# Kernel optimization log

Measured on AMD Instinct MI355X. Metric: run time of the kernel, lower is better.

Reference implementation:

```python
import jax, jax.numpy as jnp
import numpy as np

B = 256
NUM_ROUTES = 32 * 6 * 6  # 1152
NUM_CAPS = 10
OUT_CH = 16
IN_CH = 8


def squash(x, axis=-1):
    sq = jnp.sum(x * x, axis=axis, keepdims=True)
    return sq * x / ((1.0 + sq) * jnp.sqrt(sq))


def conv2d(x, w, b, stride):
    y = jax.lax.conv_general_dilated(
        x, w, window_strides=(stride, stride), padding='VALID',
        dimension_numbers=('NCHW', 'OIHW', 'NCHW'))
    return y + b[None, :, None, None]


def setup_inputs() -> dict:
    key = jax.random.key(0)
    ks = jax.random.split(key, 12)
    data = jax.random.normal(ks[0], (B, 1, 28, 28), dtype=jnp.float32)
    conv1_w = jax.random.normal(ks[1], (256, 1, 9, 9), dtype=jnp.float32) * 0.1
    conv1_b = jax.random.normal(ks[2], (256,), dtype=jnp.float32) * 0.01
    # 8 primary-capsule convs, each 256->32, k9 s2 (stacked)
    pc_w = jax.random.normal(ks[3], (8, 32, 256, 9, 9), dtype=jnp.float32) * 0.02
    pc_b = jax.random.normal(ks[4], (8, 32), dtype=jnp.float32) * 0.01
    # DigitCaps routing weights (torch.randn init)
    W_dc = jax.random.normal(ks[5], (NUM_ROUTES, NUM_CAPS, OUT_CH, IN_CH), dtype=jnp.float32)
    dec_w1 = jax.random.normal(ks[6], (160, 512), dtype=jnp.float32) * 0.05
    dec_b1 = jnp.zeros((512,), dtype=jnp.float32)
    dec_w2 = jax.random.normal(ks[7], (512, 1024), dtype=jnp.float32) * 0.05
    dec_b2 = jnp.zeros((1024,), dtype=jnp.float32)
    dec_w3 = jax.random.normal(ks[8], (1024, 784), dtype=jnp.float32) * 0.05
    dec_b3 = jnp.zeros((784,), dtype=jnp.float32)
    return dict(data=data, conv1_w=conv1_w, conv1_b=conv1_b, pc_w=pc_w, pc_b=pc_b,
                W_dc=W_dc, dec_w1=dec_w1, dec_b1=dec_b1, dec_w2=dec_w2,
                dec_b2=dec_b2, dec_w3=dec_w3, dec_b3=dec_b3)


def capsnet_forward(data, conv1_w, conv1_b, pc_w, pc_b, W_dc,
                    dec_w1, dec_b1, dec_w2, dec_b2, dec_w3, dec_b3):
    bsz = data.shape[0]
    # ConvLayer: [B,1,28,28] -> [B,256,20,20]
    x = jax.nn.relu(conv2d(data, conv1_w, conv1_b, 1))
    # PrimaryCaps: 8 independent convs fused into one 256-out conv then split
    # [B,256,6,6] viewed as [B,8,32,6,6] matches torch.stack(u, dim=1)
    u = conv2d(x, pc_w.reshape(256, 256, 9, 9), pc_b.reshape(256), 2)
    u = u.reshape(bsz, NUM_ROUTES, IN_CH)  # [B,1152,8]
    u = squash(u)
    # DigitCaps: u_hat[b,r,c,o] = sum_i W[r,c,o,i] * u[b,r,i]
    u_hat = jnp.einsum('rcoi,bri->brco', W_dc, u)  # [B,1152,10,16]
    b_ij = jnp.zeros((NUM_ROUTES, NUM_CAPS), dtype=u_hat.dtype)
    num_iterations = 3
    v = None
    for it in range(num_iterations):
        c_ij = jax.nn.softmax(b_ij, axis=0)            # softmax over routes
        s_j = jnp.einsum('rc,brco->bco', c_ij, u_hat)  # [B,10,16]
        v = squash(s_j, axis=-1)
        if it < num_iterations - 1:
            a_ij = jnp.einsum('brco,bco->rc', u_hat, v) / bsz  # mean over batch
            b_ij = b_ij + a_ij
    output = v[..., None]  # [B,10,16,1]
    # Decoder
    classes = jnp.sqrt(jnp.sum(output ** 2, axis=2))   # [B,10,1]
    classes = jax.nn.softmax(classes, axis=0)          # softmax over batch (as in source)
    idx = jnp.argmax(classes, axis=1)[:, 0]            # [B]
    masked = jnp.eye(NUM_CAPS, dtype=output.dtype)[idx]  # [B,10]
    t = (output * masked[:, :, None, None]).reshape(bsz, -1)  # [B,160]
    h = jax.nn.relu(t @ dec_w1 + dec_b1)
    h = jax.nn.relu(h @ dec_w2 + dec_b2)
    recon = jax.nn.sigmoid(h @ dec_w3 + dec_b3).reshape(bsz, 1, 28, 28)
    return output, recon, masked


def reference(data, conv1_w, conv1_b, pc_w, pc_b, W_dc,
              dec_w1, dec_b1, dec_w2, dec_b2, dec_w3, dec_b3):
    return capsnet_forward(data, conv1_w, conv1_b, pc_w, pc_b, W_dc,
                           dec_w1, dec_b1, dec_w2, dec_b2, dec_w3, dec_b3)
```

## Files before the change

### kernel.cpp

```cpp
#include <hip/hip_runtime.h>
#include <math.h>


typedef __attribute__((ext_vector_type(8))) short short8;
typedef __attribute__((ext_vector_type(4))) float f32x4;

__device__ __forceinline__ unsigned short f2bf(float x) {
  unsigned int u = __float_as_uint(x);
  unsigned int r = (u + 0x7fffu + ((u >> 16) & 1u)) >> 16;
  return (unsigned short)r;
}
__device__ __forceinline__ float bf2f(unsigned short h) {
  return __uint_as_float(((unsigned int)h) << 16);
}
__device__ __forceinline__ void gload16(const void* g, void* l) {
  __builtin_amdgcn_global_load_lds(
      (const __attribute__((address_space(1))) unsigned int*)g,
      (__attribute__((address_space(3))) unsigned int*)l, 16, 0, 0);
}
__device__ __forceinline__ float dot8(const float* w, float4 a, float4 b) {
  return w[0]*a.x + w[1]*a.y + w[2]*a.z + w[3]*a.w +
         w[4]*b.x + w[5]*b.y + w[6]*b.z + w[7]*b.w;
}

__global__ __launch_bounds__(320) void conv1_kernel(
    const float* __restrict__ data, const float* __restrict__ w1,
    const float* __restrict__ b1, unsigned short* __restrict__ xh,
    unsigned short* __restrict__ xl)
{
  const int bid = blockIdx.x;
  const int b   = bid >> 2;
  const int cog = bid & 3;
  __shared__ float img[784];
  __shared__ float wsm[81][64];
  const int t = threadIdx.x;
  for (int i = t; i < 784; i += 320) img[i] = data[b * 784 + i];
  for (int i = t; i < 64 * 81; i += 320) {
    int col = i / 81, k = i % 81;
    wsm[k][col] = w1[(cog * 64 + col) * 81 + k];
  }
  __syncthreads();
  const int cg = t & 15;
  const int oy = t >> 4;
  const int co0 = cog * 64 + cg * 4;
  float acc[4][20];
  #pragma unroll
  for (int i = 0; i < 4; i++) {
    float bv = b1[co0 + i];
    #pragma unroll
    for (int j = 0; j < 20; j++) acc[i][j] = bv;
  }
  for (int ky = 0; ky < 9; ky++) {
    float xr[28];
    const float4* rp = reinterpret_cast<const float4*>(&img[(oy + ky) * 28]);
    #pragma unroll
    for (int q = 0; q < 7; q++) {
      float4 v4 = rp[q];
      xr[q*4+0] = v4.x; xr[q*4+1] = v4.y; xr[q*4+2] = v4.z; xr[q*4+3] = v4.w;
    }
    #pragma unroll
    for (int kx = 0; kx < 9; kx++) {
      float4 wv = *reinterpret_cast<const float4*>(&wsm[ky * 9 + kx][cg * 4]);
      #pragma unroll
      for (int ox = 0; ox < 20; ox++) {
        float xv = xr[ox + kx];
        acc[0][ox] = fmaf(xv, wv.x, acc[0][ox]);
        acc[1][ox] = fmaf(xv, wv.y, acc[1][ox]);
        acc[2][ox] = fmaf(xv, wv.z, acc[2][ox]);
        acc[3][ox] = fmaf(xv, wv.w, acc[3][ox]);
      }
    }
  }
  #pragma unroll
  for (int ox = 0; ox < 20; ox++) {
    ushort4 hv, lv;
    float v0 = fmaxf(acc[0][ox], 0.f), v1 = fmaxf(acc[1][ox], 0.f);
    float v2 = fmaxf(acc[2][ox], 0.f), v3 = fmaxf(acc[3][ox], 0.f);
    hv.x = f2bf(v0); lv.x = f2bf(v0 - bf2f(hv.x));
    hv.y = f2bf(v1); lv.y = f2bf(v1 - bf2f(hv.y));
    hv.z = f2bf(v2); lv.z = f2bf(v2 - bf2f(hv.z));
    hv.w = f2bf(v3); lv.w = f2bf(v3 - bf2f(hv.w));
    const int pix = (b * 20 + oy) * 20 + ox;
    *(ushort4*)(xh + pix * 256 + co0) = hv;
    *(ushort4*)(xl + pix * 256 + co0) = lv;
  }
}

__global__ void wprep(const float* __restrict__ pw, unsigned short* __restrict__ wh,
                      unsigned short* __restrict__ wl)
{
  const int co = blockIdx.x;
  const int t  = threadIdx.x;
  __shared__ float slab[20736];
  for (int i = t; i < 20736; i += 256) slab[i] = pw[co * 20736 + i];
  __syncthreads();
  const int cc = t >> 5, ci5 = t & 31;
  for (int k = 0; k < 81; k++) {
    float x = slab[t * 81 + k];
    unsigned short h = f2bf(x);
    int dst = ((k * 8 + cc) * 256 + co) * 32 + ci5;
    wh[dst] = h;
    wl[dst] = f2bf(x - bf2f(h));
  }
}

__global__ __launch_bounds__(512) void conv2_mfma(
    const unsigned short* __restrict__ xh, const unsigned short* __restrict__ xl,
    const unsigned short* __restrict__ wh, const unsigned short* __restrict__ wl,
    float* __restrict__ part)
{
  extern __shared__ char lds[];
  const int t   = threadIdx.x;
  const int blk = blockIdx.x;
  const int mt  = blk % 72;
  const int kg  = blk / 72;
  const int m0  = mt * 128;
  const int lane = t & 63;
  const int w    = t >> 6;
  const int l15  = lane & 15, l4 = lane >> 4;
  const int mh = w >> 2, nw = w & 3;

  const int g0   = t ^ ((t >> 3) & 7);
  const int row0 = g0 >> 3, ch = g0 & 7;
  auto pixbase = [&](int pix) {
    int ab = pix / 36; int sp = pix - ab * 36;
    int oy = sp / 6;   int ox = sp - oy * 6;
    return ((ab * 20 + 2 * oy) * 20 + 2 * ox) * 256;
  };
  const int abase0 = pixbase(m0 + row0) + ch * 8;
  const int abase1 = pixbase(m0 + row0 + 64) + ch * 8;

  const int bofs = (nw * 64 + l15) * 32 + l4 * 8;

  f32x4 acc[4][4];
  #pragma unroll
  for (int i = 0; i < 4; i++)
    #pragma unroll
    for (int j = 0; j < 4; j++) acc[i][j] = (f32x4){0.f, 0.f, 0.f, 0.f};

  const int ky0 = kg * 3;

  auto stageA = [&](int buf, int xy, int ci0) {
    char* base = lds + buf * 32768;
    gload16(xh + abase0 + xy + ci0, base + t * 16);
    gload16(xh + abase1 + xy + ci0, base + 8192  + t * 16);
    gload16(xl + abase0 + xy + ci0, base + 16384 + t * 16);
    gload16(xl + abase1 + xy + ci0, base + 24576 + t * 16);
  };

  stageA(0, ky0 * 20 * 256, 0);
  int kyc = ky0, kxc = 0, cc2 = 0;
  #pragma unroll 1
  for (int s = 0; s < 108; ++s) {
    const int kkc = (kyc * 9 + kxc) * 8 + cc2 * 2;
    short8 b_h[4][2], b_l[4][2];
    #pragma unroll
    for (int ks = 0; ks < 2; ks++) {
      const unsigned short* bhp = wh + (kkc + ks) * 8192 + bofs;
      const unsigned short* blp = wl + (kkc + ks) * 8192 + bofs;
      #pragma unroll
      for (int nf = 0; nf < 4; nf++) {
        b_h[nf][ks] = *(const short8*)(bhp + nf * 512);
        b_l[nf][ks] = *(const short8*)(blp + nf * 512);
      }
    }
    cc2++; if (cc2 == 4) { cc2 = 0; kxc++; if (kxc == 9) { kxc = 0; kyc++; } }
    if (s < 107) {
      stageA((s + 1) % 3, (kyc * 20 + kxc) * 256, cc2 * 64);
      asm volatile("s_waitcnt vmcnt(20)" ::: "memory");
    } else {
      asm volatile("s_waitcnt vmcnt(16)" ::: "memory");
    }
    asm volatile("s_barrier" ::: "memory");

    char* base = lds + (s % 3) * 32768;
    #pragma unroll
    for (int ks = 0; ks < 2; ks++) {
      short8 a_h[4], a_l[4];
      #pragma unroll
      for (int mf = 0; mf < 4; mf++) {
        const int row = mh * 64 + mf * 16 + l15;
        const int off = ((row * 8 + ks * 4 + l4) ^ (row & 7)) << 4;
        a_h[mf] = *(const short8*)(base + off);
        a_l[mf] = *(const short8*)(base + 16384 + off);
      }
      __builtin_amdgcn_s_setprio(1);
      #pragma unroll
      for (int nf = 0; nf < 4; nf++)
        #pragma unroll
        for (int mf = 0; mf < 4; mf++) {
          f32x4 a = acc[mf][nf];
          a = __builtin_amdgcn_mfma_f32_16x16x32_bf16(a_h[mf], b_h[nf][ks], a, 0, 0, 0);
          a = __builtin_amdgcn_mfma_f32_16x16x32_bf16(a_l[mf], b_h[nf][ks], a, 0, 0, 0);
          a = __builtin_amdgcn_mfma_f32_16x16x32_bf16(a_h[mf], b_l[nf][ks], a, 0, 0, 0);
          acc[mf][nf] = a;
        }
      __builtin_amdgcn_s_setprio(0);
    }
  }

  float* pout = part + kg * 2359296;
  #pragma unroll
  for (int mf = 0; mf < 4; mf++)
    #pragma unroll
    for (int nf = 0; nf < 4; nf++) {
      const int co = nw * 64 + nf * 16 + l15;
      #pragma unroll
      for (int reg = 0; reg < 4; reg++) {
        const int pix = m0 + mh * 64 + mf * 16 + l4 * 4 + reg;
        const int b  = pix / 36;
        const int sp = pix - b * 36;
        pout[b * 9216 + co * 36 + sp] = acc[mf][nf][reg];
      }
    }
}

__global__ void combine_squash(const float* __restrict__ part,
                               const float* __restrict__ pb,
                               float* __restrict__ uT)
{
  const int id = blockIdx.x * 256 + threadIdx.x;
  const int b = id / 1152;
  const int r = id % 1152;
  const float* p0 = part + b * 9216 + r * 8;
  float v[8];
  #pragma unroll
  for (int i = 0; i < 8; i++) v[i] = p0[i] + p0[2359296 + i] + p0[4718592 + i];
  #pragma unroll
  for (int i = 0; i < 8; i++) v[i] += pb[(r * 8 + i) / 36];
  float sq = 0.f;
  #pragma unroll
  for (int i = 0; i < 8; i++) sq += v[i] * v[i];
  float scale = sq / ((1.f + sq) * sqrtf(sq));
  #pragma unroll
  for (int i = 0; i < 8; i++) uT[(r * 256 + b) * 8 + i] = v[i] * scale;
}

__global__ __launch_bounds__(256) void s_pass(
    const float* __restrict__ uT, const float* __restrict__ Wdc,
    const float* __restrict__ bij, float* __restrict__ spart, int uniform)
{
  const int c  = blockIdx.x % 10;
  const int q  = blockIdx.x / 10;
  const int r0 = q * 18;
  const int t  = threadIdx.x;
  __shared__ float wsm[18 * 128];
  __shared__ float cw[18];
  __shared__ float red[8];

  #pragma unroll
  for (int k = 0; k < 9; k++) {
    int idx = t + k * 256;
    int r = idx >> 7, i = idx & 127;
    wsm[idx] = Wdc[((r0 + r) * 10 + c) * 128 + i];
  }
  if (uniform) {
    if (t < 18) cw[t] = 1.f / 1152.f;
  } else {
    float bv[5]; float m = -1e30f;
    #pragma unroll
    for (int rr = 0; rr < 5; rr++) {
      int r = t + rr * 256;
      bv[rr] = (r < 1152) ? bij[c * 1152 + r] : -1e30f;
      m = fmaxf(m, bv[rr]);
    }
    #pragma unroll
    for (int off = 32; off; off >>= 1) m = fmaxf(m, __shfl_down(m, off, 64));
    if ((t & 63) == 0) red[t >> 6] = m;
    __syncthreads();
    m = fmaxf(fmaxf(red[0], red[1]), fmaxf(red[2], red[3]));
    float ssum = 0.f;
    #pragma unroll
    for (int rr = 0; rr < 5; rr++)
      ssum += (t + rr * 256 < 1152) ? expf(bv[rr] - m) : 0.f;
    #pragma unroll
    for (int off = 32; off; off >>= 1) ssum += __shfl_down(ssum, off, 64);
    if ((t & 63) == 0) red[4 + (t >> 6)] = ssum;
    __syncthreads();
    float inv = 1.f / (red[4] + red[5] + red[6] + red[7]);
    if (t < 18) cw[t] = expf(bij[c * 1152 + r0 + t] - m) * inv;
  }
  __syncthreads();

  const float4* up = (const float4*)(uT + (r0 * 256 + t) * 8);
  float acc[16];
  #pragma unroll
  for (int o = 0; o < 16; o++) acc[o] = 0.f;
  #pragma unroll 1
  for (int r = 0; r < 18; r++) {
    float4 x0 = up[r * 512], x1 = up[r * 512 + 1];
    float cwr = cw[r];
    const float* wr = &wsm[r * 128];
    #pragma unroll
    for (int o = 0; o < 16; o++) {
      const float4 wa = *(const float4*)(wr + o * 8);
      const float4 wb = *(const float4*)(wr + o * 8 + 4);
      acc[o] += cwr * (wa.x*x0.x + wa.y*x0.y + wa.z*x0.z + wa.w*x0.w
                     + wb.x*x1.x + wb.y*x1.y + wb.z*x1.z + wb.w*x1.w);
    }
  }
  float* op = spart + q * 40960 + (t * 10 + c) * 16;
  #pragma unroll
  for (int o = 0; o < 16; o++) op[o] = acc[o];
}

template <int FINAL>
__global__ void reduce_squash(const float* __restrict__ spart, float* __restrict__ outb)
{
  const int id = blockIdx.x * 256 + threadIdx.x;
  float a = 0.f;
  #pragma unroll 8
  for (int q = 0; q < 64; q++) a += spart[q * 40960 + id];
  if (FINAL) { outb[id] = a; return; }
  float sq = a * a;
  #pragma unroll
  for (int off = 8; off; off >>= 1) sq += __shfl_xor(sq, off, 16);
  float scale = sq / ((1.f + sq) * sqrtf(sq));
  const int bc = id >> 4, o = id & 15;
  const int b = bc / 10, c = bc - b * 10;
  outb[(c * 256 + b) * 16 + o] = a * scale;
}

__global__ __launch_bounds__(256) void a_pass(
    const float* __restrict__ uT, const float* __restrict__ W,
    const float* __restrict__ vT, float* __restrict__ bij, int assign)
{
  const int r = blockIdx.x;
  const int t = threadIdx.x;
  __shared__ float wsl[1280];
  __shared__ float lred[4][10];
  for (int i = t; i < 1280; i += 256) wsl[i] = W[r * 1280 + i];
  __syncthreads();
  const float4* up = (const float4*)(uT + (r * 256 + t) * 8);
  float4 ua = up[0], ub = up[1];
  const int lane = t & 63, wid = t >> 6;
  #pragma unroll 1
  for (int c = 0; c < 10; c++) {
    const float* wc = &wsl[c * 128];
    const float4* vp = (const float4*)(vT + (c * 256 + t) * 16);
    float p = 0.f;
    #pragma unroll
    for (int q = 0; q < 4; q++) {
      float4 vq = vp[q];
      p += dot8(wc + (q * 4 + 0) * 8, ua, ub) * vq.x;
      p += dot8(wc + (q * 4 + 1) * 8, ua, ub) * vq.y;
      p += dot8(wc + (q * 4 + 2) * 8, ua, ub) * vq.z;
      p += dot8(wc + (q * 4 + 3) * 8, ua, ub) * vq.w;
    }
    for (int off = 32; off; off >>= 1) p += __shfl_down(p, off, 64);
    if (lane == 0) lred[wid][c] = p;
  }
  __syncthreads();
  if (t < 10) {
    float a = (lred[0][t] + lred[1][t] + lred[2][t] + lred[3][t]) * (1.f / 256.f);
    float o = assign ? 0.f : bij[t * 1152 + r];
    bij[t * 1152 + r] = o + a;
  }
}

__global__ __launch_bounds__(256) void finalize(
    const float* __restrict__ sbuf, float* __restrict__ outp,
    float* __restrict__ maskedo, float* __restrict__ tbuf)
{
  const int b = threadIdx.x;
  __shared__ float nsm[256][10];
  __shared__ float red[8];
  #pragma unroll 1
  for (int c = 0; c < 10; c++) {
    const float4* sp = (const float4*)(sbuf + (b * 10 + c) * 16);
    float4 q0 = sp[0], q1 = sp[1], q2 = sp[2], q3 = sp[3];
    float sq = q0.x*q0.x+q0.y*q0.y+q0.z*q0.z+q0.w*q0.w
             + q1.x*q1.x+q1.y*q1.y+q1.z*q1.z+q1.w*q1.w
             + q2.x*q2.x+q2.y*q2.y+q2.z*q2.z+q2.w*q2.w
             + q3.x*q3.x+q3.y*q3.y+q3.z*q3.z+q3.w*q3.w;
    float scale = sq / ((1.f + sq) * sqrtf(sq));
    float4* op = (float4*)(outp + (b * 10 + c) * 16);
    op[0] = make_float4(q0.x*scale, q0.y*scale, q0.z*scale, q0.w*scale);
    op[1] = make_float4(q1.x*scale, q1.y*scale, q1.z*scale, q1.w*scale);
    op[2] = make_float4(q2.x*scale, q2.y*scale, q2.z*scale, q2.w*scale);
    op[3] = make_float4(q3.x*scale, q3.y*scale, q3.z*scale, q3.w*scale);
    nsm[b][c] = sq / (1.f + sq);
  }
  __syncthreads();
  float sc[10];
  #pragma unroll
  for (int c = 0; c < 10; c++) {
    float x = nsm[b][c];
    float m = x;
    #pragma unroll
    for (int off = 32; off; off >>= 1) m = fmaxf(m, __shfl_down(m, off, 64));
    if ((b & 63) == 0) red[b >> 6] = m;
    __syncthreads();
    m = fmaxf(fmaxf(red[0], red[1]), fmaxf(red[2], red[3]));
    float e = expf(x - m), ss = e;
    #pragma unroll
    for (int off = 32; off; off >>= 1) ss += __shfl_down(ss, off, 64);
    if ((b & 63) == 0) red[4 + (b >> 6)] = ss;
    __syncthreads();
    sc[c] = e / (red[4] + red[5] + red[6] + red[7]);
    __syncthreads();
  }
  int idx = 0; float best = sc[0];
  #pragma unroll
  for (int c = 1; c < 10; c++) if (sc[c] > best) { best = sc[c]; idx = c; }
  #pragma unroll
  for (int c = 0; c < 10; c++) {
    float msk = (c == idx) ? 1.f : 0.f;
    maskedo[b * 10 + c] = msk;
    const float4* op = (const float4*)(outp + (b * 10 + c) * 16);
    float4* tp = (float4*)(tbuf + b * 160 + c * 16);
    #pragma unroll
    for (int qq = 0; qq < 4; qq++) {
      float4 vv = op[qq];
      tp[qq] = make_float4(vv.x * msk, vv.y * msk, vv.z * msk, vv.w * msk);
    }
  }
}

template <int ACT>
__global__ __launch_bounds__(256) void gemm_act(
    const float* __restrict__ A, const float* __restrict__ B,
    const float* __restrict__ bias, float* __restrict__ C, int M, int N, int K)
{
  __shared__ float As[64][17];
  __shared__ float Bs[16][64];
  const int t = threadIdx.x;
  const int tx = t & 15, ty = t >> 4;
  const int m0 = blockIdx.y * 64, n0 = blockIdx.x * 64;
  float acc[4][4] = {};
  for (int kb = 0; kb < K; kb += 16) {
    {
      int row = t >> 2, c4 = (t & 3) * 4;
      float4 av = *(const float4*)(A + (m0 + row) * K + kb + c4);
      As[row][c4+0]=av.x; As[row][c4+1]=av.y; As[row][c4+2]=av.z; As[row][c4+3]=av.w;
    }
    {
      int row = t >> 4, c4 = (t & 15) * 4;
      float4 bv = make_float4(0.f, 0.f, 0.f, 0.f);
      if (n0 + c4 < N) bv = *(const float4*)(B + (kb + row) * N + n0 + c4);
      Bs[row][c4+0]=bv.x; Bs[row][c4+1]=bv.y; Bs[row][c4+2]=bv.z; Bs[row][c4+3]=bv.w;
    }
    __syncthreads();
    #pragma unroll
    for (int kk = 0; kk < 16; kk++) {
      float a_[4], b_[4];
      #pragma unroll
      for (int i = 0; i < 4; i++) a_[i] = As[ty * 4 + i][kk];
      #pragma unroll
      for (int j = 0; j < 4; j++) b_[j] = Bs[kk][tx * 4 + j];
      #pragma unroll
      for (int i = 0; i < 4; i++)
        for (int j = 0; j < 4; j++)
          acc[i][j] = fmaf(a_[i], b_[j], acc[i][j]);
    }
    __syncthreads();
  }
  #pragma unroll
  for (int i = 0; i < 4; i++) {
    int row = m0 + ty * 4 + i;
    #pragma unroll
    for (int j = 0; j < 4; j++) {
      int col = n0 + tx * 4 + j;
      if (col < N) {
        float val = acc[i][j] + bias[col];
        if (ACT == 0) val = val > 0.f ? val : 0.f;
        else          val = 1.f / (1.f + expf(-val));
        C[row * N + col] = val;
      }
    }
  }
}

extern "C" void kernel_launch(void* const* d_in, const int* in_sizes, int n_in,
                              void* d_out, int out_size, void* d_ws, size_t ws_size,
                              hipStream_t stream)
{
  const float* data = (const float*)d_in[0];
  const float* w1   = (const float*)d_in[1];
  const float* b1   = (const float*)d_in[2];
  const float* pw   = (const float*)d_in[3];
  const float* pb   = (const float*)d_in[4];
  const float* Wdc  = (const float*)d_in[5];
  const float* dw1  = (const float*)d_in[6];
  const float* db1  = (const float*)d_in[7];
  const float* dw2  = (const float*)d_in[8];
  const float* db2  = (const float*)d_in[9];
  const float* dw3  = (const float*)d_in[10];
  const float* db3  = (const float*)d_in[11];

  float* out     = (float*)d_out;
  float* outp    = out;
  float* recon   = out + 40960;
  float* maskedo = out + 241664;

  char* wsb = (char*)d_ws;
  unsigned short* x1h = (unsigned short*)(wsb);
  unsigned short* x1l = (unsigned short*)(wsb + 52428800);
  unsigned short* wbh = (unsigned short*)(wsb + 104857600);
  unsigned short* wbl = (unsigned short*)(wsb + 115474432);
  float*  part = (float*)(wsb + 126091264);
  float* uT   = (float*)(wsb);
  float* vT   = (float*)(wsb + 9437184);
  float* bij  = (float*)(wsb + 9601024);
  float* sbuf = (float*)(wsb + 9647104);
  float* spart= (float*)(wsb + 9810944);
  float* tbuf = (float*)(wsb + 20296704);
  float* h1   = (float*)(wsb + 20460544);
  float* h2   = (float*)(wsb + 20984832);

  conv1_kernel<<<1024, 320, 0, stream>>>(data, w1, b1, x1h, x1l);
  wprep<<<256, 256, 0, stream>>>(pw, wbh, wbl);
  conv2_mfma<<<216, 512, 98304, stream>>>(x1h, x1l, wbh, wbl, part);
  combine_squash<<<1152, 256, 0, stream>>>(part, pb, uT);

  s_pass<<<640, 256, 0, stream>>>(uT, Wdc, bij, spart, 1);
  reduce_squash<0><<<160, 256, 0, stream>>>(spart, vT);
  a_pass<<<1152, 256, 0, stream>>>(uT, Wdc, vT, bij, 1);
  s_pass<<<640, 256, 0, stream>>>(uT, Wdc, bij, spart, 0);
  reduce_squash<0><<<160, 256, 0, stream>>>(spart, vT);
  a_pass<<<1152, 256, 0, stream>>>(uT, Wdc, vT, bij, 0);
  s_pass<<<640, 256, 0, stream>>>(uT, Wdc, bij, spart, 0);
  reduce_squash<1><<<160, 256, 0, stream>>>(spart, sbuf);
  finalize<<<1, 256, 0, stream>>>(sbuf, outp, maskedo, tbuf);

  gemm_act<0><<<dim3(8, 4),  256, 0, stream>>>(tbuf, dw1, db1, h1,    256, 512,  160);
  gemm_act<0><<<dim3(16, 4), 256, 0, stream>>>(h1,   dw2, db2, h2,    256, 1024, 512);
  gemm_act<1><<<dim3(13, 4), 256, 0, stream>>>(h2,   dw3, db3, recon, 256, 784,  1024);
}
```

Baseline: 724.2 us.

## Split conv2 MFMA over input-channel halves and smaller M tiles for more blocks

The primary-capsule conv GEMM now uses 64-pixel tiles with 256 threads and splits the K reduction six ways (3 kernel-row groups × 2 input-channel halves), so 864 blocks launch instead of 216. The goal is to fill all CUs on the MI355X and raise occupancy through smaller static LDS per block. The cost is that the partial-sum buffer grows to six slices, which combine_squash must read and add, bringing more global traffic. Each block also reloads the B fragments for less M reuse.

```diff
diff --git a/kernel.cpp b/kernel.cpp
--- a/kernel.cpp
+++ b/kernel.cpp
@@ -104,33 +104,36 @@
   }
 }
 
-__global__ __launch_bounds__(512) void conv2_mfma(
+__global__ __launch_bounds__(256) void conv2_mfma(
     const unsigned short* __restrict__ xh, const unsigned short* __restrict__ xl,
     const unsigned short* __restrict__ wh, const unsigned short* __restrict__ wl,
     float* __restrict__ part)
 {
-  extern __shared__ char lds[];
+  __shared__ char lds[49152];
   const int t   = threadIdx.x;
   const int blk = blockIdx.x;
-  const int mt  = blk % 72;
-  const int kg  = blk / 72;
-  const int m0  = mt * 128;
+  const int mt  = blk % 144;
+  const int kg  = blk / 144;
+  const int kyg = kg % 3;
+  const int cih = kg / 3;
+  const int m0  = mt * 64;
   const int lane = t & 63;
   const int w    = t >> 6;
   const int l15  = lane & 15, l4 = lane >> 4;
-  const int mh = w >> 2, nw = w & 3;
-
-  const int g0   = t ^ ((t >> 3) & 7);
-  const int row0 = g0 >> 3, ch = g0 & 7;
+
+  const int g0  = t ^ ((t >> 3) & 7);
+  const int ar0 = g0 >> 3;
+  const int ach = g0 & 7;
   auto pixbase = [&](int pix) {
     int ab = pix / 36; int sp = pix - ab * 36;
     int oy = sp / 6;   int ox = sp - oy * 6;
     return ((ab * 20 + 2 * oy) * 20 + 2 * ox) * 256;
   };
-  const int abase0 = pixbase(m0 + row0) + ch * 8;
-  const int abase1 = pixbase(m0 + row0 + 64) + ch * 8;
-
-  const int bofs = (nw * 64 + l15) * 32 + l4 * 8;
+  const int abase0 = pixbase(m0 + ar0) + ach * 8;
+  const int abase1 = pixbase(m0 + ar0 + 32) + ach * 8;
+
+  const int bofs = (w * 64 + l15) * 32 + l4 * 8;
+  const int cibase = cih * 128;
 
   f32x4 acc[4][4];
   #pragma unroll
@@ -138,21 +141,21 @@
     #pragma unroll
     for (int j = 0; j < 4; j++) acc[i][j] = (f32x4){0.f, 0.f, 0.f, 0.f};
 
-  const int ky0 = kg * 3;
+  const int ky0 = kyg * 3;
 
   auto stageA = [&](int buf, int xy, int ci0) {
-    char* base = lds + buf * 32768;
+    char* base = lds + buf * 16384;
     gload16(xh + abase0 + xy + ci0, base + t * 16);
-    gload16(xh + abase1 + xy + ci0, base + 8192  + t * 16);
-    gload16(xl + abase0 + xy + ci0, base + 16384 + t * 16);
-    gload16(xl + abase1 + xy + ci0, base + 24576 + t * 16);
+    gload16(xh + abase1 + xy + ci0, base + 4096  + t * 16);
+    gload16(xl + abase0 + xy + ci0, base + 8192  + t * 16);
+    gload16(xl + abase1 + xy + ci0, base + 12288 + t * 16);
   };
 
-  stageA(0, ky0 * 20 * 256, 0);
+  stageA(0, ky0 * 20 * 256, cibase);
   int kyc = ky0, kxc = 0, cc2 = 0;
   #pragma unroll 1
-  for (int s = 0; s < 108; ++s) {
-    const int kkc = (kyc * 9 + kxc) * 8 + cc2 * 2;
+  for (int s = 0; s < 54; ++s) {
+    const int kkc = (kyc * 9 + kxc) * 8 + cih * 4 + cc2 * 2;
     short8 b_h[4][2], b_l[4][2];
     #pragma unroll
     for (int ks = 0; ks < 2; ks++) {
@@ -164,25 +167,25 @@
         b_l[nf][ks] = *(const short8*)(blp + nf * 512);
       }
     }
-    cc2++; if (cc2 == 4) { cc2 = 0; kxc++; if (kxc == 9) { kxc = 0; kyc++; } }
-    if (s < 107) {
-      stageA((s + 1) % 3, (kyc * 20 + kxc) * 256, cc2 * 64);
+    cc2++; if (cc2 == 2) { cc2 = 0; kxc++; if (kxc == 9) { kxc = 0; kyc++; } }
+    if (s < 53) {
+      stageA((s + 1) % 3, (kyc * 20 + kxc) * 256, cibase + cc2 * 64);
       asm volatile("s_waitcnt vmcnt(20)" ::: "memory");
     } else {
       asm volatile("s_waitcnt vmcnt(16)" ::: "memory");
     }
     asm volatile("s_barrier" ::: "memory");
 
-    char* base = lds + (s % 3) * 32768;
+    char* base = lds + (s % 3) * 16384;
     #pragma unroll
     for (int ks = 0; ks < 2; ks++) {
       short8 a_h[4], a_l[4];
       #pragma unroll
       for (int mf = 0; mf < 4; mf++) {
-        const int row = mh * 64 + mf * 16 + l15;
-        const int off = ((row * 8 + ks * 4 + l4) ^ (row & 7)) << 4;
+        const int row = mf * 16 + l15;
+        const int off = ((row * 8 + ks * 4 + l4) ^ (l15 & 7)) << 4;
         a_h[mf] = *(const short8*)(base + off);
-        a_l[mf] = *(const short8*)(base + 16384 + off);
+        a_l[mf] = *(const short8*)(base + 8192 + off);
       }
       __builtin_amdgcn_s_setprio(1);
       #pragma unroll
@@ -204,10 +207,10 @@
   for (int mf = 0; mf < 4; mf++)
     #pragma unroll
     for (int nf = 0; nf < 4; nf++) {
-      const int co = nw * 64 + nf * 16 + l15;
+      const int co = w * 64 + nf * 16 + l15;
       #pragma unroll
       for (int reg = 0; reg < 4; reg++) {
-        const int pix = m0 + mh * 64 + mf * 16 + l4 * 4 + reg;
+        const int pix = m0 + mf * 16 + l4 * 4 + reg;
         const int b  = pix / 36;
         const int sp = pix - b * 36;
         pout[b * 9216 + co * 36 + sp] = acc[mf][nf][reg];
@@ -225,7 +228,9 @@
   const float* p0 = part + b * 9216 + r * 8;
   float v[8];
   #pragma unroll
-  for (int i = 0; i < 8; i++) v[i] = p0[i] + p0[2359296 + i] + p0[4718592 + i];
+  for (int i = 0; i < 8; i++)
+    v[i] = ((p0[i] + p0[2359296 + i]) + (p0[4718592 + i] + p0[7077888 + i]))
+         + (p0[9437184 + i] + p0[11796480 + i]);
   #pragma unroll
   for (int i = 0; i < 8; i++) v[i] += pb[(r * 8 + i) / 36];
   float sq = 0.f;
@@ -510,7 +515,7 @@
 
   conv1_kernel<<<1024, 320, 0, stream>>>(data, w1, b1, x1h, x1l);
   wprep<<<256, 256, 0, stream>>>(pw, wbh, wbl);
-  conv2_mfma<<<216, 512, 98304, stream>>>(x1h, x1l, wbh, wbl, part);
+  conv2_mfma<<<864, 256, 0, stream>>>(x1h, x1l, wbh, wbl, part);
   combine_squash<<<1152, 256, 0, stream>>>(part, pb, uT);
 
   s_pass<<<640, 256, 0, stream>>>(uT, Wdc, bij, spart, 1);
```

Result: faster. 706.7 us (-2.4%).

## Split conv2 reduction over input-channel halves to double block count

Applied to the files above, without the earlier changes.

The primary-capsule conv GEMM now splits K six ways (three ky groups times two channel halves) instead of three, doubling the grid so more CUs are occupied. Each block runs half as many K steps with a double-buffered LDS pipeline in place of triple buffering. The combine kernel now sums six partial slices. The cost is extra partial-sum memory traffic, less prefetch depth, and a larger workspace footprint.

```diff
diff --git a/kernel.cpp b/kernel.cpp
--- a/kernel.cpp
+++ b/kernel.cpp
@@ -109,11 +109,13 @@
     const unsigned short* __restrict__ wh, const unsigned short* __restrict__ wl,
     float* __restrict__ part)
 {
-  extern __shared__ char lds[];
+  __shared__ char lds[65536];
   const int t   = threadIdx.x;
   const int blk = blockIdx.x;
-  const int mt  = blk % 72;
-  const int kg  = blk / 72;
+  const int mt  = blk / 6;
+  const int kg  = blk % 6;
+  const int kyg = kg % 3;
+  const int cih = kg / 3;
   const int m0  = mt * 128;
   const int lane = t & 63;
   const int w    = t >> 6;
@@ -121,16 +123,18 @@
   const int mh = w >> 2, nw = w & 3;
 
   const int g0   = t ^ ((t >> 3) & 7);
-  const int row0 = g0 >> 3, ch = g0 & 7;
+  const int ar0  = g0 >> 3;
+  const int ach  = g0 & 7;
   auto pixbase = [&](int pix) {
     int ab = pix / 36; int sp = pix - ab * 36;
     int oy = sp / 6;   int ox = sp - oy * 6;
     return ((ab * 20 + 2 * oy) * 20 + 2 * ox) * 256;
   };
-  const int abase0 = pixbase(m0 + row0) + ch * 8;
-  const int abase1 = pixbase(m0 + row0 + 64) + ch * 8;
+  const int abase0 = pixbase(m0 + ar0) + ach * 8;
+  const int abase1 = pixbase(m0 + 64 + ar0) + ach * 8;
 
   const int bofs = (nw * 64 + l15) * 32 + l4 * 8;
+  const int cibase = cih * 128;
 
   f32x4 acc[4][4];
   #pragma unroll
@@ -138,7 +142,7 @@
     #pragma unroll
     for (int j = 0; j < 4; j++) acc[i][j] = (f32x4){0.f, 0.f, 0.f, 0.f};
 
-  const int ky0 = kg * 3;
+  const int ky0 = kyg * 3;
 
   auto stageA = [&](int buf, int xy, int ci0) {
     char* base = lds + buf * 32768;
@@ -148,11 +152,11 @@
     gload16(xl + abase1 + xy + ci0, base + 24576 + t * 16);
   };
 
-  stageA(0, ky0 * 20 * 256, 0);
+  stageA(0, ky0 * 20 * 256, cibase);
   int kyc = ky0, kxc = 0, cc2 = 0;
   #pragma unroll 1
-  for (int s = 0; s < 108; ++s) {
-    const int kkc = (kyc * 9 + kxc) * 8 + cc2 * 2;
+  for (int s = 0; s < 54; ++s) {
+    const int kkc = (kyc * 9 + kxc) * 8 + cih * 4 + cc2 * 2;
     short8 b_h[4][2], b_l[4][2];
     #pragma unroll
     for (int ks = 0; ks < 2; ks++) {
@@ -164,25 +168,21 @@
         b_l[nf][ks] = *(const short8*)(blp + nf * 512);
       }
     }
-    cc2++; if (cc2 == 4) { cc2 = 0; kxc++; if (kxc == 9) { kxc = 0; kyc++; } }
-    if (s < 107) {
-      stageA((s + 1) % 3, (kyc * 20 + kxc) * 256, cc2 * 64);
-      asm volatile("s_waitcnt vmcnt(20)" ::: "memory");
-    } else {
-      asm volatile("s_waitcnt vmcnt(16)" ::: "memory");
-    }
+    asm volatile("s_waitcnt vmcnt(16)" ::: "memory");
     asm volatile("s_barrier" ::: "memory");
-
-    char* base = lds + (s % 3) * 32768;
+    cc2++; if (cc2 == 2) { cc2 = 0; kxc++; if (kxc == 9) { kxc = 0; kyc++; } }
+    if (s < 53) stageA((s + 1) & 1, (kyc * 20 + kxc) * 256, cibase + cc2 * 64);
+
+    char* base = lds + (s & 1) * 32768;
     #pragma unroll
     for (int ks = 0; ks < 2; ks++) {
       short8 a_h[4], a_l[4];
       #pragma unroll
       for (int mf = 0; mf < 4; mf++) {
-        const int row = mh * 64 + mf * 16 + l15;
-        const int off = ((row * 8 + ks * 4 + l4) ^ (row & 7)) << 4;
-        a_h[mf] = *(const short8*)(base + off);
-        a_l[mf] = *(const short8*)(base + 16384 + off);
+        const int rr  = mf * 16 + l15;
+        const int off = (((rr << 3) | (ks * 4 + l4)) ^ (rr & 7)) << 4;
+        a_h[mf] = *(const short8*)(base + mh * 8192 + off);
+        a_l[mf] = *(const short8*)(base + 16384 + mh * 8192 + off);
       }
       __builtin_amdgcn_s_setprio(1);
       #pragma unroll
@@ -225,7 +225,9 @@
   const float* p0 = part + b * 9216 + r * 8;
   float v[8];
   #pragma unroll
-  for (int i = 0; i < 8; i++) v[i] = p0[i] + p0[2359296 + i] + p0[4718592 + i];
+  for (int i = 0; i < 8; i++)
+    v[i] = ((p0[i] + p0[2359296 + i]) + (p0[4718592 + i] + p0[7077888 + i]))
+         + (p0[9437184 + i] + p0[11796480 + i]);
   #pragma unroll
   for (int i = 0; i < 8; i++) v[i] += pb[(r * 8 + i) / 36];
   float sq = 0.f;
@@ -510,7 +512,7 @@
 
   conv1_kernel<<<1024, 320, 0, stream>>>(data, w1, b1, x1h, x1l);
   wprep<<<256, 256, 0, stream>>>(pw, wbh, wbl);
-  conv2_mfma<<<216, 512, 98304, stream>>>(x1h, x1l, wbh, wbl, part);
+  conv2_mfma<<<432, 512, 0, stream>>>(x1h, x1l, wbh, wbl, part);
   combine_squash<<<1152, 256, 0, stream>>>(part, pb, uT);
 
   s_pass<<<640, 256, 0, stream>>>(uT, Wdc, bij, spart, 1);
```

New measurement: 776.9 us. 7.3% more time.
